# Kernel tuning notes

Hardware: AMD Instinct MI355X
Metric: run time of the kernel (lower is better)

Reference implementation:

```python
import jax, jax.numpy as jnp
import numpy as np

N_NODES = 100000
N_EDGES = 1600000
D = 128
BN_EPS = 1e-5

def setup_inputs() -> dict:
    key = jax.random.key(0)
    ks = jax.random.split(key, 6)
    h = jax.random.normal(ks[0], (N_NODES, D), dtype=jnp.float32)
    src = jax.random.randint(ks[1], (N_EDGES,), 0, N_NODES, dtype=jnp.int32)
    dst = jax.random.randint(ks[2], (N_EDGES,), 0, N_NODES, dtype=jnp.int32)
    eps = jnp.zeros((1,), dtype=jnp.float32)
    # 2-layer GIN apply_func MLP, scaled for stable activations
    W1 = jax.random.normal(ks[3], (D, D), dtype=jnp.float32) / np.sqrt(D)
    b1 = jnp.zeros((D,), dtype=jnp.float32)
    W2 = jax.random.normal(ks[4], (D, D), dtype=jnp.float32) / np.sqrt(D)
    b2 = jnp.zeros((D,), dtype=jnp.float32)
    gamma = jnp.ones((D,), dtype=jnp.float32)
    beta = jnp.zeros((D,), dtype=jnp.float32)
    return {"h": h, "src": src, "dst": dst, "eps": eps,
            "W1": W1, "b1": b1, "W2": W2, "b2": b2,
            "gamma": gamma, "beta": beta}

def reference(h, src, dst, eps, W1, b1, W2, b2, gamma, beta):
    # --- neighbor sum aggregation: update_all(copy_u('h'), fn.sum) ---
    msgs = h[src]                                   # [E, D] irregular gather
    neigh = jax.ops.segment_sum(msgs, dst, num_segments=N_NODES)  # [N, D]
    # --- eps-scaled self term ---
    x = (1.0 + eps[0]) * h + neigh                  # [N, D]
    # --- apply_func: 2-layer MLP ---
    x = jax.nn.relu(x @ W1 + b1)
    x = x @ W2 + b2
    # --- BatchNorm1d over node dim (training-mode batch stats) ---
    mean = jnp.mean(x, axis=0)
    var = jnp.mean(jnp.square(x - mean), axis=0)
    x = (x - mean) * jax.lax.rsqrt(var + BN_EPS) * gamma + beta
    # --- activation + residual ---
    x = jax.nn.relu(x)
    x = h + x  # residual (in_dim == out_dim)
    return x
```

## Files before the change

### kernel.cpp

```cpp
#include <hip/hip_runtime.h>

#define NN 100000
#define NE 1600000
#define DD 128
#define BN_EPS 1e-5f

#define NWIN 782
#define EPB 8192
#define NBLK ((NE + EPB - 1) / EPB)
#define CAP 3072
#define PREPBLKS 316
#define GRID_PS (NBLK + PREPBLKS)
#define BN_BLOCKS 1024

typedef __attribute__((ext_vector_type(8))) short short8;
typedef __attribute__((ext_vector_type(4))) float floatx4;

__device__ __forceinline__ unsigned short f2bf(float f) {
    union { float f; unsigned u; } v; v.f = f;
    return (unsigned short)((v.u + 0x7FFFu + ((v.u >> 16) & 1u)) >> 16);
}
__device__ __forceinline__ float bf2f(unsigned short u) {
    union { unsigned u; float f; } v; v.u = ((unsigned)u) << 16;
    return v.f;
}

__global__ __launch_bounds__(256) void prep_scatter_kernel(
    float* __restrict__ stats,
    const float* __restrict__ W1, const float* __restrict__ W2,
    unsigned short* __restrict__ W1t, unsigned short* __restrict__ W2t,
    const float* __restrict__ h, unsigned short* __restrict__ hb, int do_hb,
    const int* __restrict__ src, const int* __restrict__ dst,
    int* __restrict__ wcnt, int* __restrict__ estage)
{
    __shared__ int bins[NWIN];
    __shared__ int dstl[EPB];
    int t = threadIdx.x;

    if (blockIdx.x < NBLK) {
        int blk = blockIdx.x;
        for (int j = t; j < NWIN; j += 256) bins[j] = 0;
        __syncthreads();
        int base = blk * EPB;
        int cnt = min(EPB, NE - base);
        for (int i = t; i < cnt; i += 256) {
            int d = dst[base + i];
            dstl[i] = d;
            atomicAdd(&bins[d >> 7], 1);
        }
        __syncthreads();
        for (int j = t; j < NWIN; j += 256) {
            int c = bins[j];
            int b = (c > 0) ? atomicAdd(&wcnt[j], c) : 0;
            bins[j] = j * CAP + b;
        }
        __syncthreads();
        for (int i = t; i < cnt; i += 256) {
            int d = dstl[i];
            int pos = atomicAdd(&bins[d >> 7], 1);
            estage[pos] = (src[base + i] << 7) | (d & 127);
        }
    } else {
        int tid0 = (blockIdx.x - NBLK) * 256 + t;
        int stride = PREPBLKS * 256;
        if (tid0 < 2 * DD) stats[tid0] = 0.0f;
        for (int i = tid0; i < DD * DD; i += stride) {
            int n = i >> 7, k = i & 127;
            W1t[i] = f2bf(W1[k * DD + n]);
            W2t[i] = f2bf(W2[k * DD + n]);
        }
        if (do_hb) {
            const float4* h4 = (const float4*)h;
            ushort4* hb4 = (ushort4*)hb;
            for (int i = tid0; i < NN * (DD / 4); i += stride) {
                float4 v = h4[i];
                ushort4 o;
                o.x = f2bf(v.x); o.y = f2bf(v.y); o.z = f2bf(v.z); o.w = f2bf(v.w);
                hb4[i] = o;
            }
        }
    }
}

template <bool HB>
__global__ __launch_bounds__(512) void permgather_kernel(
    const float* __restrict__ h, const unsigned short* __restrict__ hb,
    const float* __restrict__ eps, const int* __restrict__ wcnt,
    const int* __restrict__ estage, unsigned short* __restrict__ xb)
{
    __shared__ int ew[CAP];
    __shared__ int es[CAP];
    __shared__ int cnt[128];
    __shared__ int scn[128];
    __shared__ int begS[128];
    __shared__ int endS[128];
    __shared__ int cur[128];

    int b = blockIdx.x, t = threadIdx.x;
    if (t < 128) cnt[t] = 0;
    __syncthreads();

    int n = min(wcnt[b], CAP);
    int wbase = b * CAP;
    for (int i = t; i < n; i += 512) {
        int e = estage[wbase + i];
        ew[i] = e;
        atomicAdd(&cnt[e & 127], 1);
    }
    __syncthreads();

    if (t < 128) scn[t] = cnt[t];
    __syncthreads();
#pragma unroll
    for (int ofs = 1; ofs < 128; ofs <<= 1) {
        int u = (t < 128 && t >= ofs) ? scn[t - ofs] : 0;
        __syncthreads();
        if (t < 128) scn[t] += u;
        __syncthreads();
    }
    if (t < 128) {
        int excl = scn[t] - cnt[t];
        begS[t] = excl;
        endS[t] = excl + cnt[t];
        cur[t] = excl;
    }
    __syncthreads();

    for (int i = t; i < n; i += 512) {
        int e = ew[i];
        int pos = atomicAdd(&cur[e & 127], 1);
        es[pos] = e >> 7;
    }
    __syncthreads();

    const float sE = 1.0f + eps[0];
    const float4* h4 = (const float4*)h;
    const short8* hb8 = (const short8*)hb;
    int c8 = t & 15;
#pragma unroll
    for (int pass = 0; pass < 4; ++pass) {
        int nl = pass * 32 + (t >> 4);
        int node = (b << 7) + nl;
        if (node >= NN) continue;
        float4 a0 = h4[node * 32 + c8 * 2];
        float4 a1 = h4[node * 32 + c8 * 2 + 1];
        float acc[8] = {sE * a0.x, sE * a0.y, sE * a0.z, sE * a0.w,
                        sE * a1.x, sE * a1.y, sE * a1.z, sE * a1.w};
        int e = begS[nl], eend = endS[nl];
        if (HB) {
            for (; e + 3 < eend; e += 4) {
                int s0 = es[e], s1 = es[e + 1], s2 = es[e + 2], s3 = es[e + 3];
                short8 v0 = hb8[s0 * 16 + c8];
                short8 v1 = hb8[s1 * 16 + c8];
                short8 v2 = hb8[s2 * 16 + c8];
                short8 v3 = hb8[s3 * 16 + c8];
#pragma unroll
                for (int j = 0; j < 8; ++j) {
                    float t0 = bf2f((unsigned short)v0[j]) + bf2f((unsigned short)v1[j]);
                    float t1 = bf2f((unsigned short)v2[j]) + bf2f((unsigned short)v3[j]);
                    acc[j] += t0 + t1;
                }
            }
            for (; e < eend; ++e) {
                short8 v0 = hb8[es[e] * 16 + c8];
#pragma unroll
                for (int j = 0; j < 8; ++j) acc[j] += bf2f((unsigned short)v0[j]);
            }
        } else {
            for (; e + 1 < eend; e += 2) {
                int s0 = es[e], s1 = es[e + 1];
                float4 u0 = h4[s0 * 32 + c8 * 2], u1 = h4[s0 * 32 + c8 * 2 + 1];
                float4 w0 = h4[s1 * 32 + c8 * 2], w1 = h4[s1 * 32 + c8 * 2 + 1];
                acc[0] += u0.x + w0.x; acc[1] += u0.y + w0.y;
                acc[2] += u0.z + w0.z; acc[3] += u0.w + w0.w;
                acc[4] += u1.x + w1.x; acc[5] += u1.y + w1.y;
                acc[6] += u1.z + w1.z; acc[7] += u1.w + w1.w;
            }
            if (e < eend) {
                int s0 = es[e];
                float4 u0 = h4[s0 * 32 + c8 * 2], u1 = h4[s0 * 32 + c8 * 2 + 1];
                acc[0] += u0.x; acc[1] += u0.y; acc[2] += u0.z; acc[3] += u0.w;
                acc[4] += u1.x; acc[5] += u1.y; acc[6] += u1.z; acc[7] += u1.w;
            }
        }
        short8 o;
#pragma unroll
        for (int j = 0; j < 8; ++j) o[j] = (short)f2bf(acc[j]);
        ((short8*)xb)[node * 16 + c8] = o;
    }
}

__global__ __launch_bounds__(256) void mlp_fused_kernel(
    const unsigned short* __restrict__ X,
    const unsigned short* __restrict__ W1t, const unsigned short* __restrict__ W2t,
    const float* __restrict__ b1, const float* __restrict__ b2,
    unsigned short* __restrict__ Y, float* __restrict__ stats)
{
    extern __shared__ char smem[];
    unsigned short* wl = (unsigned short*)smem;
    unsigned short* xl = (unsigned short*)(smem + 34816);

    const int tid = threadIdx.x;
    const int r0 = blockIdx.x * 64;
    const int lane = tid & 63;
    const int wv = tid >> 6;
    const int m = lane & 15;
    const int hi = lane >> 4;

    const short8* W18 = (const short8*)W1t;
#pragma unroll
    for (int l = 0; l < 8; ++l) {
        int idx = tid + l * 256;
        int n = idx >> 4, c = idx & 15;
        *(short8*)&wl[n * 136 + c * 8] = W18[idx];
    }
    const short8* X8 = (const short8*)X;
#pragma unroll
    for (int l = 0; l < 4; ++l) {
        int idx = tid + l * 256;
        int row = idx >> 4, c = idx & 15;
        int g = r0 + row;
        short8 v = {0, 0, 0, 0, 0, 0, 0, 0};
        if (g < NN) v = X8[g * 16 + c];
        *(short8*)&xl[row * 136 + c * 8] = v;
    }
    __syncthreads();

    floatx4 acc[8];
#pragma unroll
    for (int i = 0; i < 8; ++i) acc[i] = (floatx4){0.f, 0.f, 0.f, 0.f};
#pragma unroll
    for (int kc = 0; kc < 4; ++kc) {
        short8 a = *(const short8*)&xl[(wv * 16 + m) * 136 + kc * 32 + hi * 8];
#pragma unroll
        for (int nt = 0; nt < 8; ++nt) {
            short8 b = *(const short8*)&wl[(nt * 16 + m) * 136 + kc * 32 + hi * 8];
            acc[nt] = __builtin_amdgcn_mfma_f32_16x16x32_bf16(a, b, acc[nt], 0, 0, 0);
        }
    }
    __syncthreads();

#pragma unroll
    for (int nt = 0; nt < 8; ++nt) {
        float bv = b1[nt * 16 + m];
#pragma unroll
        for (int r = 0; r < 4; ++r) {
            float v = fmaxf(acc[nt][r] + bv, 0.f);
            xl[(wv * 16 + hi * 4 + r) * 136 + nt * 16 + m] = f2bf(v);
        }
    }
    const short8* W28 = (const short8*)W2t;
#pragma unroll
    for (int l = 0; l < 8; ++l) {
        int idx = tid + l * 256;
        int n = idx >> 4, c = idx & 15;
        *(short8*)&wl[n * 136 + c * 8] = W28[idx];
    }
    __syncthreads();

#pragma unroll
    for (int i = 0; i < 8; ++i) acc[i] = (floatx4){0.f, 0.f, 0.f, 0.f};
#pragma unroll
    for (int kc = 0; kc < 4; ++kc) {
        short8 a = *(const short8*)&xl[(wv * 16 + m) * 136 + kc * 32 + hi * 8];
#pragma unroll
        for (int nt = 0; nt < 8; ++nt) {
            short8 b = *(const short8*)&wl[(nt * 16 + m) * 136 + kc * 32 + hi * 8];
            acc[nt] = __builtin_amdgcn_mfma_f32_16x16x32_bf16(a, b, acc[nt], 0, 0, 0);
        }
    }
    __syncthreads();

#pragma unroll
    for (int nt = 0; nt < 8; ++nt) {
        float bv = b2[nt * 16 + m];
#pragma unroll
        for (int r = 0; r < 4; ++r) {
            float v = acc[nt][r] + bv;
            xl[(wv * 16 + hi * 4 + r) * 136 + nt * 16 + m] = f2bf(v);
        }
    }
    __syncthreads();

#pragma unroll
    for (int l = 0; l < 4; ++l) {
        int idx = tid + l * 256;
        int row = idx >> 4, c = idx & 15;
        int g = r0 + row;
        if (g < NN)
            ((short8*)Y)[g * 16 + c] = *(const short8*)&xl[row * 136 + c * 8];
    }

    int col = tid & 127, half = tid >> 7;
    int rlim = min(64, NN - r0);
    int rbeg = half * 32, rend = min(rbeg + 32, rlim);
    float s = 0.f, q = 0.f;
    for (int r = rbeg; r < rend; ++r) {
        float v = bf2f(xl[r * 136 + col]);
        s += v; q += v * v;
    }
    float* red = (float*)wl;
    red[tid] = s;
    red[256 + tid] = q;
    __syncthreads();
    if (half == 0) {
        atomicAdd(&stats[col],      red[col] + red[128 + col]);
        atomicAdd(&stats[DD + col], red[256 + col] + red[256 + 128 + col]);
    }
}

__global__ __launch_bounds__(256) void bn_final_kernel(
    const unsigned short* __restrict__ Y, const float* __restrict__ h,
    const float* __restrict__ gamma, const float* __restrict__ beta,
    const float* __restrict__ stats, float* __restrict__ out)
{
    const float invN = 1.0f / (float)NN;
    int t0 = blockIdx.x * 256 + threadIdx.x;
    int c8 = t0 & 15;
    float sc[8], sh[8];
#pragma unroll
    for (int j = 0; j < 8; ++j) {
        int col = c8 * 8 + j;
        float mu = stats[col] * invN;
        float var = stats[DD + col] * invN - mu * mu;
        float s = rsqrtf(var + BN_EPS) * gamma[col];
        sc[j] = s;
        sh[j] = beta[col] - mu * s;
    }
    const short8* Y8 = (const short8*)Y;
    const float4* H4 = (const float4*)h;
    float4* O4 = (float4*)out;
    const int total = NN * 16;
    const int stride = BN_BLOCKS * 256;
    for (int i = t0; i < total; i += stride) {
        short8 u = Y8[i];
        float4 h0 = H4[2 * i], h1 = H4[2 * i + 1];
        float4 r0, r1;
        r0.x = h0.x + fmaxf(bf2f((unsigned short)u[0]) * sc[0] + sh[0], 0.f);
        r0.y = h0.y + fmaxf(bf2f((unsigned short)u[1]) * sc[1] + sh[1], 0.f);
        r0.z = h0.z + fmaxf(bf2f((unsigned short)u[2]) * sc[2] + sh[2], 0.f);
        r0.w = h0.w + fmaxf(bf2f((unsigned short)u[3]) * sc[3] + sh[3], 0.f);
        r1.x = h1.x + fmaxf(bf2f((unsigned short)u[4]) * sc[4] + sh[4], 0.f);
        r1.y = h1.y + fmaxf(bf2f((unsigned short)u[5]) * sc[5] + sh[5], 0.f);
        r1.z = h1.z + fmaxf(bf2f((unsigned short)u[6]) * sc[6] + sh[6], 0.f);
        r1.w = h1.w + fmaxf(bf2f((unsigned short)u[7]) * sc[7] + sh[7], 0.f);
        O4[2 * i] = r0;
        O4[2 * i + 1] = r1;
    }
}

extern "C" void kernel_launch(void* const* d_in, const int* in_sizes, int n_in,
                              void* d_out, int out_size, void* d_ws, size_t ws_size,
                              hipStream_t stream)
{
    const float* h     = (const float*)d_in[0];
    const int*   src   = (const int*)d_in[1];
    const int*   dst   = (const int*)d_in[2];
    const float* eps   = (const float*)d_in[3];
    const float* W1    = (const float*)d_in[4];
    const float* b1    = (const float*)d_in[5];
    const float* W2    = (const float*)d_in[6];
    const float* b2    = (const float*)d_in[7];
    const float* gamma = (const float*)d_in[8];
    const float* beta  = (const float*)d_in[9];
    float* out = (float*)d_out;

    char* w = (char*)d_ws;
    size_t o = 0;
    float* stats    = (float*)(w + o); o += 256 * 4;
    int* wcnt       = (int*)(w + o); o += 1024 * 4;
    unsigned short* W1t = (unsigned short*)(w + o); o += (size_t)DD * DD * 2;
    unsigned short* W2t = (unsigned short*)(w + o); o += (size_t)DD * DD * 2;
    int* estage     = (int*)(w + o); o += (size_t)NWIN * CAP * 4;
    unsigned short* xb  = (unsigned short*)(w + o); o += (size_t)NN * DD * 2;
    unsigned short* hb  = (unsigned short*)(w + o); o += (size_t)NN * DD * 2;
    const int use_hb = (ws_size >= o) ? 1 : 0;

    hipMemsetAsync(wcnt, 0, 1024 * sizeof(int), stream);

    prep_scatter_kernel<<<GRID_PS, 256, 0, stream>>>(
        stats, W1, W2, W1t, W2t, h, hb, use_hb, src, dst, wcnt, estage);

    if (use_hb)
        permgather_kernel<true><<<NWIN, 512, 0, stream>>>(h, hb, eps, wcnt, estage, xb);
    else
        permgather_kernel<false><<<NWIN, 512, 0, stream>>>(h, hb, eps, wcnt, estage, xb);

    int gemm_blocks = (NN + 63) / 64;
    size_t gemm_lds = 34816 + 17408;
    mlp_fused_kernel<<<gemm_blocks, 256, gemm_lds, stream>>>(xb, W1t, W2t, b1, b2, xb, stats);

    bn_final_kernel<<<BN_BLOCKS, 256, 0, stream>>>(xb, h, gamma, beta, stats, out);
}
```

Before: 298.2 us.

## Locally sort edges per window before scatter and degree-order gather nodes

The scatter phase now computes per-block window offsets with a prefix scan, sorts edges into shared memory by window, and then writes each window's run contiguously to the global staging buffer. This replaces scattered atomically-positioned global stores with sequential runs. The gather kernel drops to 256 threads, removes the staging copy in shared memory, and processes the nodes of each window in degree-sorted order so that the 16-lane groups in a wavefront have similar edge counts, reducing divergence. More prep blocks are launched for the weight and h conversion. The extra scans and syncs add overhead, and the per-window copy loop is serial per thread.

```diff
diff --git a/kernel.cpp b/kernel.cpp
--- a/kernel.cpp
+++ b/kernel.cpp
@@ -6,10 +6,11 @@
 #define BN_EPS 1e-5f
 
 #define NWIN 782
+#define NWINP 1024
 #define EPB 8192
 #define NBLK ((NE + EPB - 1) / EPB)
 #define CAP 3072
-#define PREPBLKS 316
+#define PREPBLKS 828
 #define GRID_PS (NBLK + PREPBLKS)
 #define BN_BLOCKS 1024
 
@@ -33,32 +34,65 @@
     const int* __restrict__ src, const int* __restrict__ dst,
     int* __restrict__ wcnt, int* __restrict__ estage)
 {
-    __shared__ int bins[NWIN];
-    __shared__ int dstl[EPB];
+    __shared__ int lofs[NWINP];
+    __shared__ int lcur[NWINP];
+    __shared__ int gbase[NWINP];
+    __shared__ int sorted[EPB];
+    __shared__ int stmp[256];
     int t = threadIdx.x;
 
     if (blockIdx.x < NBLK) {
         int blk = blockIdx.x;
-        for (int j = t; j < NWIN; j += 256) bins[j] = 0;
+        for (int w = t; w < NWINP; w += 256) lcur[w] = 0;
         __syncthreads();
         int base = blk * EPB;
         int cnt = min(EPB, NE - base);
+        for (int i = t; i < cnt; i += 256)
+            atomicAdd(&lcur[dst[base + i] >> 7], 1);
+        __syncthreads();
+
+        int w0 = t * 4;
+        int c0 = lcur[w0], c1 = lcur[w0 + 1], c2 = lcur[w0 + 2], c3 = lcur[w0 + 3];
+        int tsum = c0 + c1 + c2 + c3;
+        stmp[t] = tsum;
+        __syncthreads();
+#pragma unroll
+        for (int ofs = 1; ofs < 256; ofs <<= 1) {
+            int u = (t >= ofs) ? stmp[t - ofs] : 0;
+            __syncthreads();
+            stmp[t] += u;
+            __syncthreads();
+        }
+        int excl = stmp[t] - tsum;
+        lofs[w0]     = excl;
+        lofs[w0 + 1] = excl + c0;
+        lofs[w0 + 2] = excl + c0 + c1;
+        lofs[w0 + 3] = excl + c0 + c1 + c2;
+        int gb0 = (w0     < NWIN && c0) ? atomicAdd(&wcnt[w0],     c0) : 0;
+        int gb1 = (w0 + 1 < NWIN && c1) ? atomicAdd(&wcnt[w0 + 1], c1) : 0;
+        int gb2 = (w0 + 2 < NWIN && c2) ? atomicAdd(&wcnt[w0 + 2], c2) : 0;
+        int gb3 = (w0 + 3 < NWIN && c3) ? atomicAdd(&wcnt[w0 + 3], c3) : 0;
+        gbase[w0]     = w0 * CAP + gb0;
+        gbase[w0 + 1] = (w0 + 1) * CAP + gb1;
+        gbase[w0 + 2] = (w0 + 2) * CAP + gb2;
+        gbase[w0 + 3] = (w0 + 3) * CAP + gb3;
+        lcur[w0] = lofs[w0]; lcur[w0 + 1] = lofs[w0 + 1];
+        lcur[w0 + 2] = lofs[w0 + 2]; lcur[w0 + 3] = lofs[w0 + 3];
+        __syncthreads();
+
         for (int i = t; i < cnt; i += 256) {
             int d = dst[base + i];
-            dstl[i] = d;
-            atomicAdd(&bins[d >> 7], 1);
-        }
-        __syncthreads();
-        for (int j = t; j < NWIN; j += 256) {
-            int c = bins[j];
-            int b = (c > 0) ? atomicAdd(&wcnt[j], c) : 0;
-            bins[j] = j * CAP + b;
-        }
-        __syncthreads();
-        for (int i = t; i < cnt; i += 256) {
-            int d = dstl[i];
-            int pos = atomicAdd(&bins[d >> 7], 1);
-            estage[pos] = (src[base + i] << 7) | (d & 127);
+            int s = src[base + i];
+            int p = atomicAdd(&lcur[d >> 7], 1);
+            sorted[p] = (s << 7) | (d & 127);
+        }
+        __syncthreads();
+
+        for (int w = t; w < NWIN; w += 256) {
+            int lb = lofs[w], le = lcur[w];
+            int g = gbase[w];
+            for (int j = lb; j < le; ++j)
+                estage[g + (j - lb)] = sorted[j];
         }
     } else {
         int tid0 = (blockIdx.x - NBLK) * 256 + t;
@@ -83,53 +117,68 @@
 }
 
 template <bool HB>
-__global__ __launch_bounds__(512) void permgather_kernel(
+__global__ __launch_bounds__(256) void permgather_kernel(
     const float* __restrict__ h, const unsigned short* __restrict__ hb,
     const float* __restrict__ eps, const int* __restrict__ wcnt,
     const int* __restrict__ estage, unsigned short* __restrict__ xb)
 {
-    __shared__ int ew[CAP];
     __shared__ int es[CAP];
     __shared__ int cnt[128];
-    __shared__ int scn[128];
-    __shared__ int begS[128];
-    __shared__ int endS[128];
+    __shared__ int beg[128];
     __shared__ int cur[128];
+    __shared__ int dh[64];
+    __shared__ int dcur[64];
+    __shared__ unsigned char order[128];
 
     int b = blockIdx.x, t = threadIdx.x;
     if (t < 128) cnt[t] = 0;
+    if (t < 64) dh[t] = 0;
     __syncthreads();
 
     int n = min(wcnt[b], CAP);
     int wbase = b * CAP;
-    for (int i = t; i < n; i += 512) {
+    for (int i = t; i < n; i += 256)
+        atomicAdd(&cnt[estage[wbase + i] & 127], 1);
+    __syncthreads();
+
+    if (t < 128) beg[t] = cnt[t];
+    __syncthreads();
+#pragma unroll
+    for (int ofs = 1; ofs < 128; ofs <<= 1) {
+        int u = (t < 128 && t >= ofs) ? beg[t - ofs] : 0;
+        __syncthreads();
+        if (t < 128) beg[t] += u;
+        __syncthreads();
+    }
+    if (t < 128) {
+        int ex = beg[t] - cnt[t];
+        beg[t] = ex;
+        cur[t] = ex;
+        atomicAdd(&dh[min(cnt[t], 63)], 1);
+    }
+    __syncthreads();
+
+    if (t < 64) dcur[t] = dh[t];
+    __syncthreads();
+#pragma unroll
+    for (int ofs = 1; ofs < 64; ofs <<= 1) {
+        int u = (t < 64 && t >= ofs) ? dcur[t - ofs] : 0;
+        __syncthreads();
+        if (t < 64) dcur[t] += u;
+        __syncthreads();
+    }
+    if (t < 64) dcur[t] -= dh[t];
+    __syncthreads();
+    if (t < 128) {
+        int p = atomicAdd(&dcur[min(cnt[t], 63)], 1);
+        order[p] = (unsigned char)t;
+    }
+    __syncthreads();
+
+    for (int i = t; i < n; i += 256) {
         int e = estage[wbase + i];
-        ew[i] = e;
-        atomicAdd(&cnt[e & 127], 1);
-    }
-    __syncthreads();
-
-    if (t < 128) scn[t] = cnt[t];
-    __syncthreads();
-#pragma unroll
-    for (int ofs = 1; ofs < 128; ofs <<= 1) {
-        int u = (t < 128 && t >= ofs) ? scn[t - ofs] : 0;
-        __syncthreads();
-        if (t < 128) scn[t] += u;
-        __syncthreads();
-    }
-    if (t < 128) {
-        int excl = scn[t] - cnt[t];
-        begS[t] = excl;
-        endS[t] = excl + cnt[t];
-        cur[t] = excl;
-    }
-    __syncthreads();
-
-    for (int i = t; i < n; i += 512) {
-        int e = ew[i];
-        int pos = atomicAdd(&cur[e & 127], 1);
-        es[pos] = e >> 7;
+        int p = atomicAdd(&cur[e & 127], 1);
+        es[p] = e >> 7;
     }
     __syncthreads();
 
@@ -138,15 +187,15 @@
     const short8* hb8 = (const short8*)hb;
     int c8 = t & 15;
 #pragma unroll
-    for (int pass = 0; pass < 4; ++pass) {
-        int nl = pass * 32 + (t >> 4);
+    for (int pass = 0; pass < 8; ++pass) {
+        int nl = order[pass * 16 + (t >> 4)];
         int node = (b << 7) + nl;
         if (node >= NN) continue;
         float4 a0 = h4[node * 32 + c8 * 2];
         float4 a1 = h4[node * 32 + c8 * 2 + 1];
         float acc[8] = {sE * a0.x, sE * a0.y, sE * a0.z, sE * a0.w,
                         sE * a1.x, sE * a1.y, sE * a1.z, sE * a1.w};
-        int e = begS[nl], eend = endS[nl];
+        int e = beg[nl], eend = beg[nl] + cnt[nl];
         if (HB) {
             for (; e + 3 < eend; e += 4) {
                 int s0 = es[e], s1 = es[e + 1], s2 = es[e + 2], s3 = es[e + 3];
@@ -382,9 +431,9 @@
         stats, W1, W2, W1t, W2t, h, hb, use_hb, src, dst, wcnt, estage);
 
     if (use_hb)
-        permgather_kernel<true><<<NWIN, 512, 0, stream>>>(h, hb, eps, wcnt, estage, xb);
+        permgather_kernel<true><<<NWIN, 256, 0, stream>>>(h, hb, eps, wcnt, estage, xb);
     else
-        permgather_kernel<false><<<NWIN, 512, 0, stream>>>(h, hb, eps, wcnt, estage, xb);
+        permgather_kernel<false><<<NWIN, 256, 0, stream>>>(h, hb, eps, wcnt, estage, xb);
 
     int gemm_blocks = (NN + 63) / 64;
     size_t gemm_lds = 34816 + 17408;
```

After: 296.6 us. Within noise of the previous version (-0.6%).

## Split permute and gather into separate kernels with coarser 512-node superbins

Applied to the files above, without the earlier changes.

Edges are bucketed into 512-node superbins instead of 128-node windows, so the scatter kernel needs only a 256-entry LDS histogram and no staged dst copy. A separate permute kernel sorts each superbin in place by destination and writes per-node edge offsets. The gather then runs as its own fine-grained kernel, 16 nodes per block, to raise occupancy and balance load across many more blocks. In exchange it adds a kernel launch and an extra pass over the edge buffer through global memory.

```diff
diff --git a/kernel.cpp b/kernel.cpp
--- a/kernel.cpp
+++ b/kernel.cpp
@@ -5,11 +5,13 @@
 #define DD 128
 #define BN_EPS 1e-5f
 
-#define NWIN 782
+#define SBSH 9
+#define SBSZ 512
+#define NSB ((NN + SBSZ - 1) / SBSZ)
+#define CAPS 9216
 #define EPB 8192
 #define NBLK ((NE + EPB - 1) / EPB)
-#define CAP 3072
-#define PREPBLKS 316
+#define PREPBLKS 828
 #define GRID_PS (NBLK + PREPBLKS)
 #define BN_BLOCKS 1024
 
@@ -26,44 +28,36 @@
 }
 
 __global__ __launch_bounds__(256) void prep_scatter_kernel(
-    float* __restrict__ stats,
     const float* __restrict__ W1, const float* __restrict__ W2,
     unsigned short* __restrict__ W1t, unsigned short* __restrict__ W2t,
     const float* __restrict__ h, unsigned short* __restrict__ hb, int do_hb,
     const int* __restrict__ src, const int* __restrict__ dst,
-    int* __restrict__ wcnt, int* __restrict__ estage)
-{
-    __shared__ int bins[NWIN];
-    __shared__ int dstl[EPB];
+    int* __restrict__ scnt, int* __restrict__ sbuf)
+{
+    __shared__ int bins[256];
     int t = threadIdx.x;
 
     if (blockIdx.x < NBLK) {
-        int blk = blockIdx.x;
-        for (int j = t; j < NWIN; j += 256) bins[j] = 0;
-        __syncthreads();
-        int base = blk * EPB;
-        int cnt = min(EPB, NE - base);
-        for (int i = t; i < cnt; i += 256) {
+        bins[t] = 0;
+        __syncthreads();
+        int base = blockIdx.x * EPB;
+        int ecnt = min(EPB, NE - base);
+        for (int i = t; i < ecnt; i += 256)
+            atomicAdd(&bins[dst[base + i] >> SBSH], 1);
+        __syncthreads();
+        int c = bins[t];
+        int gb = (t < NSB && c) ? atomicAdd(&scnt[t], c) : 0;
+        __syncthreads();
+        bins[t] = t * CAPS + gb;
+        __syncthreads();
+        for (int i = t; i < ecnt; i += 256) {
             int d = dst[base + i];
-            dstl[i] = d;
-            atomicAdd(&bins[d >> 7], 1);
-        }
-        __syncthreads();
-        for (int j = t; j < NWIN; j += 256) {
-            int c = bins[j];
-            int b = (c > 0) ? atomicAdd(&wcnt[j], c) : 0;
-            bins[j] = j * CAP + b;
-        }
-        __syncthreads();
-        for (int i = t; i < cnt; i += 256) {
-            int d = dstl[i];
-            int pos = atomicAdd(&bins[d >> 7], 1);
-            estage[pos] = (src[base + i] << 7) | (d & 127);
+            int p = atomicAdd(&bins[d >> SBSH], 1);
+            sbuf[p] = (src[base + i] << SBSH) | (d & (SBSZ - 1));
         }
     } else {
         int tid0 = (blockIdx.x - NBLK) * 256 + t;
         int stride = PREPBLKS * 256;
-        if (tid0 < 2 * DD) stats[tid0] = 0.0f;
         for (int i = tid0; i < DD * DD; i += stride) {
             int n = i >> 7, k = i & 127;
             W1t[i] = f2bf(W1[k * DD + n]);
@@ -82,112 +76,123 @@
     }
 }
 
-template <bool HB>
-__global__ __launch_bounds__(512) void permgather_kernel(
-    const float* __restrict__ h, const unsigned short* __restrict__ hb,
-    const float* __restrict__ eps, const int* __restrict__ wcnt,
-    const int* __restrict__ estage, unsigned short* __restrict__ xb)
-{
-    __shared__ int ew[CAP];
-    __shared__ int es[CAP];
-    __shared__ int cnt[128];
-    __shared__ int scn[128];
-    __shared__ int begS[128];
-    __shared__ int endS[128];
-    __shared__ int cur[128];
-
-    int b = blockIdx.x, t = threadIdx.x;
-    if (t < 128) cnt[t] = 0;
-    __syncthreads();
-
-    int n = min(wcnt[b], CAP);
-    int wbase = b * CAP;
+__global__ __launch_bounds__(512) void permute_kernel(
+    const int* __restrict__ scnt, int* __restrict__ sbuf,
+    int2* __restrict__ off2)
+{
+    __shared__ int ew[CAPS];
+    __shared__ int cnt[SBSZ];
+    __shared__ int cur[SBSZ];
+    __shared__ int stmp[512];
+    int sb = blockIdx.x, t = threadIdx.x;
+    cnt[t] = 0;
+    __syncthreads();
+    int n = min(scnt[sb], CAPS);
+    int sbase = sb * CAPS;
     for (int i = t; i < n; i += 512) {
-        int e = estage[wbase + i];
+        int e = sbuf[sbase + i];
         ew[i] = e;
-        atomicAdd(&cnt[e & 127], 1);
-    }
-    __syncthreads();
-
-    if (t < 128) scn[t] = cnt[t];
-    __syncthreads();
-#pragma unroll
-    for (int ofs = 1; ofs < 128; ofs <<= 1) {
-        int u = (t < 128 && t >= ofs) ? scn[t - ofs] : 0;
-        __syncthreads();
-        if (t < 128) scn[t] += u;
-        __syncthreads();
-    }
-    if (t < 128) {
-        int excl = scn[t] - cnt[t];
-        begS[t] = excl;
-        endS[t] = excl + cnt[t];
-        cur[t] = excl;
-    }
-    __syncthreads();
-
+        atomicAdd(&cnt[e & (SBSZ - 1)], 1);
+    }
+    __syncthreads();
+    int c = cnt[t];
+    stmp[t] = c;
+    __syncthreads();
+#pragma unroll
+    for (int ofs = 1; ofs < 512; ofs <<= 1) {
+        int u = (t >= ofs) ? stmp[t - ofs] : 0;
+        __syncthreads();
+        stmp[t] += u;
+        __syncthreads();
+    }
+    int excl = stmp[t] - c;
+    cur[t] = excl;
+    off2[sb * SBSZ + t] = make_int2(sbase + excl, sbase + excl + c);
+    __syncthreads();
     for (int i = t; i < n; i += 512) {
         int e = ew[i];
-        int pos = atomicAdd(&cur[e & 127], 1);
-        es[pos] = e >> 7;
-    }
-    __syncthreads();
-
-    const float sE = 1.0f + eps[0];
+        int p = atomicAdd(&cur[e & (SBSZ - 1)], 1);
+        sbuf[sbase + p] = e >> SBSH;
+    }
+}
+
+__global__ __launch_bounds__(256) void gather_bf16_kernel(
+    const float* __restrict__ h, const unsigned short* __restrict__ hb,
+    const float* __restrict__ eps, const int2* __restrict__ off2,
+    const int* __restrict__ srcs, unsigned short* __restrict__ xb)
+{
+    int node = blockIdx.x * 16 + (threadIdx.x >> 4);
+    if (node >= NN) return;
+    int c8 = threadIdx.x & 15;
+    const float s = 1.0f + eps[0];
     const float4* h4 = (const float4*)h;
+    float4 a0 = h4[node * 32 + c8 * 2];
+    float4 a1 = h4[node * 32 + c8 * 2 + 1];
+    float acc[8] = {s * a0.x, s * a0.y, s * a0.z, s * a0.w,
+                    s * a1.x, s * a1.y, s * a1.z, s * a1.w};
+    int2 oo = off2[node];
+    int e = oo.x, eend = oo.y;
     const short8* hb8 = (const short8*)hb;
-    int c8 = t & 15;
-#pragma unroll
-    for (int pass = 0; pass < 4; ++pass) {
-        int nl = pass * 32 + (t >> 4);
-        int node = (b << 7) + nl;
-        if (node >= NN) continue;
-        float4 a0 = h4[node * 32 + c8 * 2];
-        float4 a1 = h4[node * 32 + c8 * 2 + 1];
-        float acc[8] = {sE * a0.x, sE * a0.y, sE * a0.z, sE * a0.w,
-                        sE * a1.x, sE * a1.y, sE * a1.z, sE * a1.w};
-        int e = begS[nl], eend = endS[nl];
-        if (HB) {
-            for (; e + 3 < eend; e += 4) {
-                int s0 = es[e], s1 = es[e + 1], s2 = es[e + 2], s3 = es[e + 3];
-                short8 v0 = hb8[s0 * 16 + c8];
-                short8 v1 = hb8[s1 * 16 + c8];
-                short8 v2 = hb8[s2 * 16 + c8];
-                short8 v3 = hb8[s3 * 16 + c8];
-#pragma unroll
-                for (int j = 0; j < 8; ++j) {
-                    float t0 = bf2f((unsigned short)v0[j]) + bf2f((unsigned short)v1[j]);
-                    float t1 = bf2f((unsigned short)v2[j]) + bf2f((unsigned short)v3[j]);
-                    acc[j] += t0 + t1;
-                }
-            }
-            for (; e < eend; ++e) {
-                short8 v0 = hb8[es[e] * 16 + c8];
-#pragma unroll
-                for (int j = 0; j < 8; ++j) acc[j] += bf2f((unsigned short)v0[j]);
-            }
-        } else {
-            for (; e + 1 < eend; e += 2) {
-                int s0 = es[e], s1 = es[e + 1];
-                float4 u0 = h4[s0 * 32 + c8 * 2], u1 = h4[s0 * 32 + c8 * 2 + 1];
-                float4 w0 = h4[s1 * 32 + c8 * 2], w1 = h4[s1 * 32 + c8 * 2 + 1];
-                acc[0] += u0.x + w0.x; acc[1] += u0.y + w0.y;
-                acc[2] += u0.z + w0.z; acc[3] += u0.w + w0.w;
-                acc[4] += u1.x + w1.x; acc[5] += u1.y + w1.y;
-                acc[6] += u1.z + w1.z; acc[7] += u1.w + w1.w;
-            }
-            if (e < eend) {
-                int s0 = es[e];
-                float4 u0 = h4[s0 * 32 + c8 * 2], u1 = h4[s0 * 32 + c8 * 2 + 1];
-                acc[0] += u0.x; acc[1] += u0.y; acc[2] += u0.z; acc[3] += u0.w;
-                acc[4] += u1.x; acc[5] += u1.y; acc[6] += u1.z; acc[7] += u1.w;
-            }
-        }
-        short8 o;
-#pragma unroll
-        for (int j = 0; j < 8; ++j) o[j] = (short)f2bf(acc[j]);
-        ((short8*)xb)[node * 16 + c8] = o;
-    }
+    for (; e + 3 < eend; e += 4) {
+        int s0 = srcs[e],     s1 = srcs[e + 1];
+        int s2 = srcs[e + 2], s3 = srcs[e + 3];
+        short8 v0 = hb8[s0 * 16 + c8];
+        short8 v1 = hb8[s1 * 16 + c8];
+        short8 v2 = hb8[s2 * 16 + c8];
+        short8 v3 = hb8[s3 * 16 + c8];
+#pragma unroll
+        for (int j = 0; j < 8; ++j) {
+            float t0 = bf2f((unsigned short)v0[j]) + bf2f((unsigned short)v1[j]);
+            float t1 = bf2f((unsigned short)v2[j]) + bf2f((unsigned short)v3[j]);
+            acc[j] += t0 + t1;
+        }
+    }
+    for (; e < eend; ++e) {
+        short8 v0 = hb8[srcs[e] * 16 + c8];
+#pragma unroll
+        for (int j = 0; j < 8; ++j) acc[j] += bf2f((unsigned short)v0[j]);
+    }
+    short8 o;
+#pragma unroll
+    for (int j = 0; j < 8; ++j) o[j] = (short)f2bf(acc[j]);
+    ((short8*)xb)[node * 16 + c8] = o;
+}
+
+__global__ __launch_bounds__(256) void gather_f32_kernel(
+    const float* __restrict__ h, const float* __restrict__ eps,
+    const int2* __restrict__ off2, const int* __restrict__ srcs,
+    unsigned short* __restrict__ xb)
+{
+    int node = blockIdx.x * 16 + (threadIdx.x >> 4);
+    if (node >= NN) return;
+    int c8 = threadIdx.x & 15;
+    const float4* h4 = (const float4*)h;
+    const float s = 1.0f + eps[0];
+    float4 a0 = h4[node * 32 + c8 * 2];
+    float4 a1 = h4[node * 32 + c8 * 2 + 1];
+    float acc[8] = {s * a0.x, s * a0.y, s * a0.z, s * a0.w,
+                    s * a1.x, s * a1.y, s * a1.z, s * a1.w};
+    int2 oo = off2[node];
+    int e = oo.x, eend = oo.y;
+    for (; e + 1 < eend; e += 2) {
+        int s0 = srcs[e], s1 = srcs[e + 1];
+        float4 u0 = h4[s0 * 32 + c8 * 2], u1 = h4[s0 * 32 + c8 * 2 + 1];
+        float4 w0 = h4[s1 * 32 + c8 * 2], w1 = h4[s1 * 32 + c8 * 2 + 1];
+        acc[0] += u0.x + w0.x; acc[1] += u0.y + w0.y;
+        acc[2] += u0.z + w0.z; acc[3] += u0.w + w0.w;
+        acc[4] += u1.x + w1.x; acc[5] += u1.y + w1.y;
+        acc[6] += u1.z + w1.z; acc[7] += u1.w + w1.w;
+    }
+    if (e < eend) {
+        int s0 = srcs[e];
+        float4 u0 = h4[s0 * 32 + c8 * 2], u1 = h4[s0 * 32 + c8 * 2 + 1];
+        acc[0] += u0.x; acc[1] += u0.y; acc[2] += u0.z; acc[3] += u0.w;
+        acc[4] += u1.x; acc[5] += u1.y; acc[6] += u1.z; acc[7] += u1.w;
+    }
+    short8 o;
+#pragma unroll
+    for (int j = 0; j < 8; ++j) o[j] = (short)f2bf(acc[j]);
+    ((short8*)xb)[node * 16 + c8] = o;
 }
 
 __global__ __launch_bounds__(256) void mlp_fused_kernel(
@@ -368,27 +373,30 @@
     char* w = (char*)d_ws;
     size_t o = 0;
     float* stats    = (float*)(w + o); o += 256 * 4;
-    int* wcnt       = (int*)(w + o); o += 1024 * 4;
+    int* scnt       = (int*)(w + o); o += 256 * 4;
     unsigned short* W1t = (unsigned short*)(w + o); o += (size_t)DD * DD * 2;
     unsigned short* W2t = (unsigned short*)(w + o); o += (size_t)DD * DD * 2;
-    int* estage     = (int*)(w + o); o += (size_t)NWIN * CAP * 4;
+    int2* off2      = (int2*)(w + o); o += (size_t)NSB * SBSZ * 8;
+    int* sbuf       = (int*)(w + o); o += (size_t)NSB * CAPS * 4;
     unsigned short* xb  = (unsigned short*)(w + o); o += (size_t)NN * DD * 2;
     unsigned short* hb  = (unsigned short*)(w + o); o += (size_t)NN * DD * 2;
     const int use_hb = (ws_size >= o) ? 1 : 0;
 
-    hipMemsetAsync(wcnt, 0, 1024 * sizeof(int), stream);
+    hipMemsetAsync(stats, 0, 512 * sizeof(int), stream);
 
     prep_scatter_kernel<<<GRID_PS, 256, 0, stream>>>(
-        stats, W1, W2, W1t, W2t, h, hb, use_hb, src, dst, wcnt, estage);
+        W1, W2, W1t, W2t, h, hb, use_hb, src, dst, scnt, sbuf);
+
+    permute_kernel<<<NSB, 512, 0, stream>>>(scnt, sbuf, off2);
 
     if (use_hb)
-        permgather_kernel<true><<<NWIN, 512, 0, stream>>>(h, hb, eps, wcnt, estage, xb);
+        gather_bf16_kernel<<<(NN + 15) / 16, 256, 0, stream>>>(h, hb, eps, off2, sbuf, xb);
     else
-        permgather_kernel<false><<<NWIN, 512, 0, stream>>>(h, hb, eps, wcnt, estage, xb);
-
-    int gemm_blocks = (NN + 63) / 64;
+        gather_f32_kernel<<<(NN + 15) / 16, 256, 0, stream>>>(h, eps, off2, sbuf, xb);
+
     size_t gemm_lds = 34816 + 17408;
-    mlp_fused_kernel<<<gemm_blocks, 256, gemm_lds, stream>>>(xb, W1t, W2t, b1, b2, xb, stats);
+    mlp_fused_kernel<<<(NN + 63) / 64, 256, gemm_lds, stream>>>(
+        xb, W1t, W2t, b1, b2, xb, stats);
 
     bn_final_kernel<<<BN_BLOCKS, 256, 0, stream>>>(xb, h, gamma, beta, stats, out);
 }
```

New measurement: 304.2 us. +2.0%, slower.
